# Kernel optimization log

Hardware: AMD Instinct MI355X
Metric: run time of the kernel (lower is better)

Reference implementation:

```python
import jax, jax.numpy as jnp
import numpy as np

B, N, H, E, OBS, A, AFF, EFF = 2, 50000, 64, 1_000_000, 128, 18, 512, 256


def setup_inputs() -> dict:
    key = jax.random.key(0)
    ks = jax.random.split(key, 20)
    s = 0.05  # small init to keep gates/tanh unsaturated
    return {
        "obs": jax.random.normal(ks[0], (B, OBS), jnp.float32),
        "state": jax.random.normal(ks[1], (B, N, H), jnp.float32) * 0.1,
        "W_in": jax.random.normal(ks[2], (OBS, H), jnp.float32) * s,
        "b_in": jnp.zeros((H,), jnp.float32),
        "W_msg": jax.random.normal(ks[3], (H, H), jnp.float32) * s,
        "W_gate": jax.random.normal(ks[4], (2 * H, H), jnp.float32) * s,
        "b_gate": jnp.zeros((H,), jnp.float32),
        "W_cand": jax.random.normal(ks[5], (2 * H, H), jnp.float32) * s,
        "b_cand": jnp.zeros((H,), jnp.float32),
        "W_dec": jax.random.normal(ks[6], (H, H), jnp.float32) * s,
        "b_dec": jnp.zeros((H,), jnp.float32),
        "W_mean": jax.random.normal(ks[7], (H, A), jnp.float32) * s,
        "b_mean": jnp.zeros((A,), jnp.float32),
        "W_ls": jax.random.normal(ks[8], (H, A), jnp.float32) * s,
        "b_ls": jnp.zeros((A,), jnp.float32),
        "src_index": jax.random.randint(ks[9], (E,), 0, N),
        "dst_index": jax.random.randint(ks[10], (E,), 0, N),
        "afferent_idx": jax.random.randint(ks[11], (AFF,), 0, N),
        "efferent_idx": jax.random.randint(ks[12], (EFF,), 0, N),
    }


def reference(obs, state, W_in, b_in, W_msg, W_gate, b_gate, W_cand, b_cand,
              W_dec, b_dec, W_mean, b_mean, W_ls, b_ls,
              src_index, dst_index, afferent_idx, efferent_idx):
    # inject obs projection into afferent node slots
    projected = obs @ W_in + b_in                                   # [B, H]
    injected = jnp.zeros_like(state).at[:, afferent_idx, :].set(projected[:, None, :])
    # gather-project-scatter message passing over the edge list
    src_msgs = state[:, src_index, :] @ W_msg                       # [B, E, H]
    messages = jnp.zeros_like(state).at[:, dst_index, :].add(src_msgs)
    # GRU-style gated update
    combined = messages + injected
    gate_in = jnp.concatenate([state, combined], axis=-1)           # [B, N, 2H]
    z = jax.nn.sigmoid(gate_in @ W_gate + b_gate)
    cand = jnp.tanh(gate_in @ W_cand + b_cand)
    next_state = (1.0 - z) * state + z * cand
    # mean-pool readout over efferent nodes, then policy heads
    readout = next_state[:, efferent_idx, :].mean(axis=1)           # [B, H]
    decoded = jnp.tanh(readout @ W_dec + b_dec)
    mean = decoded @ W_mean + b_mean
    log_std = jnp.clip(decoded @ W_ls + b_ls, -5.0, 2.0)
    return mean, log_std, next_state
```

## Files before the change

kernel.cpp:

```cpp
#include <hip/hip_runtime.h>
#include <hip/hip_bf16.h>

constexpr int kN   = 50000;
constexpr int kH   = 64;
constexpr int kB   = 2;
constexpr int kE   = 1000000;
constexpr int kObs = 128;
constexpr int kA   = 18;
constexpr int kAff = 512;
constexpr int kEff = 256;
constexpr int kNH  = kN * kH;
constexpr int kOutOff = 2 * kB * kA;
constexpr int kRanges = 8;
constexpr int kNr  = kN / kRanges;
constexpr int kChunks = 64;
constexpr int kEc  = kE / kChunks;
constexpr int kHistB = kRanges * kChunks;
constexpr int kPackBlocks = (kNH + 8191) / 8192;
constexpr int kWprepBlocks = 20;
constexpr int kScanB = (kN + 1023) / 1024;

typedef __attribute__((ext_vector_type(8))) short short8_t;
typedef __attribute__((ext_vector_type(4))) float f32x4_t;

__device__ __forceinline__ float ldf(const void* p, int i, int f32) {
  if (f32) return ((const float*)p)[i];
  unsigned short u = ((const unsigned short*)p)[i];
  union { unsigned int x; float f; } v; v.x = ((unsigned int)u) << 16; return v.f;
}
__device__ __forceinline__ void stf(void* p, int i, float val, int f32) {
  if (f32) ((float*)p)[i] = val;
  else ((__hip_bfloat16*)p)[i] = __float2bfloat16(val);
}
__device__ __forceinline__ float lo16(unsigned int w) {
  union { unsigned int i; float f; } v; v.i = w << 16; return v.f;
}
__device__ __forceinline__ float hi16(unsigned int w) {
  union { unsigned int i; float f; } v; v.i = w & 0xffff0000u; return v.f;
}
__device__ __forceinline__ unsigned int f2b(float f) {
  union { float f; unsigned int u; } v; v.f = f;
  unsigned int r = v.u + 0x7fffu + ((v.u >> 16) & 1u);
  return r >> 16;
}
__device__ __forceinline__ int detect64(const unsigned short* wprobe, int t) {
  int hits = 0;
  for (int k = 0; k < 4; ++k) {
    unsigned short u = wprobe[(t * 4 + k) * 2];
    int e = (u >> 7) & 0xFF;
    if ((u & 0x7FFFu) != 0 && e >= 108 && e <= 128) hits++;
  }
  for (int off = 32; off; off >>= 1) hits += __shfl_down(hits, off);
  return (hits < 128) ? 1 : 0;
}

extern "C" __global__ __launch_bounds__(1024) void k_prep(
    const unsigned short* __restrict__ wprobe,
    const void* __restrict__ obs,
    const void* __restrict__ W_in,
    const void* __restrict__ b_in,
    const int* __restrict__ aff_idx,
    const int* __restrict__ dst,
    const void* __restrict__ W_msg,
    const void* __restrict__ W_gate,
    const void* __restrict__ W_cand,
    int* __restrict__ dflag,
    int* __restrict__ flags,
    float* __restrict__ projected,
    int* __restrict__ deg_c,
    unsigned short* __restrict__ wt) {
  __shared__ int sdeg[kNr];
  int t = threadIdx.x, b = blockIdx.x;
  if (b == 0) {
    __shared__ int sflag;
    if (t < 64) { int f = detect64(wprobe, t); if (t == 0) { sflag = f; dflag[0] = f; } }
    __syncthreads();
    int f32 = sflag;
    if (t < kAff) flags[aff_idx[t]] = 1;
    if (t < kB * kH) {
      int bb = t >> 6, h = t & 63;
      float acc = ldf(b_in, h, f32);
      for (int o = 0; o < kObs; ++o)
        acc += ldf(obs, bb * kObs + o, f32) * ldf(W_in, o * kH + h, f32);
      projected[t] = acc;
    }
  } else if (b <= kHistB) {
    int h = b - 1, r = h & 7, c = h >> 3;
    int r0 = r * kNr;
    for (int i = t; i < kNr; i += 1024) sdeg[i] = 0;
    __syncthreads();
    int end = (c + 1) * kEc;
    for (int e = c * kEc + t; e < end; e += 1024) {
      unsigned rel = (unsigned)(dst[e] - r0);
      if (rel < (unsigned)kNr) atomicAdd(&sdeg[rel], 1);
    }
    __syncthreads();
    for (int i = t; i < kNr; i += 1024) deg_c[c * kN + r0 + i] = sdeg[i];
  } else {
    __shared__ int sflag;
    if (t < 64) { int f = detect64(wprobe, t); if (t == 0) sflag = f; }
    __syncthreads();
    int f32 = sflag;
    int i = (b - 1 - kHistB) * 1024 + t;
    if (i < 4096) {
      int n = i >> 6, k = i & 63;
      wt[i] = (unsigned short)f2b(ldf(W_msg, k * 64 + n, f32));
    } else if (i < 12288) {
      int j = i - 4096; int n = j >> 7, k = j & 127;
      wt[i] = (unsigned short)f2b(ldf(W_gate, k * 64 + n, f32));
    } else if (i < 20480) {
      int j = i - 12288; int n = j >> 7, k = j & 127;
      wt[i] = (unsigned short)f2b(ldf(W_cand, k * 64 + n, f32));
    }
  }
}

extern "C" __global__ void k_scan1(const int* __restrict__ deg_c,
                                   int* __restrict__ row_off,
                                   int* __restrict__ partials) {
  __shared__ int sd[256];
  int t = threadIdx.x;
  int base = blockIdx.x * 1024 + t * 4;
  int d[4];
#pragma unroll
  for (int k = 0; k < 4; ++k) {
    int idx = base + k, s = 0;
    if (idx < kN) {
      for (int r = 0; r < kChunks; ++r) s += deg_c[r * kN + idx];
    }
    d[k] = s;
  }
  int s4 = d[0] + d[1] + d[2] + d[3];
  sd[t] = s4;
  __syncthreads();
  for (int off = 1; off < 256; off <<= 1) {
    int v = (t >= off) ? sd[t - off] : 0;
    __syncthreads();
    sd[t] += v;
    __syncthreads();
  }
  int excl = sd[t] - s4;
  if (t == 255) partials[blockIdx.x] = sd[255];
#pragma unroll
  for (int k = 0; k < 4; ++k) {
    if (base + k < kN) row_off[base + k] = excl;
    excl += d[k];
  }
}

extern "C" __global__ void k_scan3(int* __restrict__ row_off,
                                   const int* __restrict__ partials,
                                   int* __restrict__ deg_c) {
  __shared__ int sd[256];
  int t = threadIdx.x;
  int chunk = blockIdx.x >> 2;
  int s = 0;
  for (int j = t; j < chunk; j += 256) s += partials[j];
  sd[t] = s;
  __syncthreads();
  for (int off = 128; off; off >>= 1) {
    if (t < off) sd[t] += sd[t + off];
    __syncthreads();
  }
  int base = sd[0];
  int i = blockIdx.x * 256 + t;
  if (i < kN) {
    int v = row_off[i] + base;
    row_off[i] = v;
    int run = v;
#pragma unroll 8
    for (int c = 0; c < kChunks; ++c) {
      int d = deg_c[c * kN + i];
      deg_c[c * kN + i] = run;
      run += d;
    }
  }
  if (blockIdx.x == 0 && t == 0) row_off[kN] = kE;
}

extern "C" __global__ __launch_bounds__(1024) void k_scatter(
    const int* __restrict__ src,
    const int* __restrict__ dst,
    const int* __restrict__ chunk_base,
    int* __restrict__ sorted_src,
    const unsigned short* __restrict__ wprobe,
    const void* __restrict__ state,
    unsigned int* __restrict__ pack) {
  __shared__ int scur[kNr];
  int t = threadIdx.x;
  if (blockIdx.x < kHistB) {
    int r = blockIdx.x & 7, c = blockIdx.x >> 3;
    int r0 = r * kNr;
    for (int i = t; i < kNr; i += 1024) scur[i] = chunk_base[c * kN + r0 + i];
    __syncthreads();
    int end = (c + 1) * kEc;
    for (int e = c * kEc + t; e < end; e += 1024) {
      unsigned rel = (unsigned)(dst[e] - r0);
      if (rel < (unsigned)kNr) {
        int pos = atomicAdd(&scur[rel], 1);
        sorted_src[pos] = src[e];
      }
    }
  } else {
    __shared__ int sflag;
    if (t < 64) { int f = detect64(wprobe, t); if (t == 0) sflag = f; }
    __syncthreads();
    int f32 = sflag;
    int i = (blockIdx.x - kHistB) * 8192 + t * 8;
    if (i < kNH) {
      uint4 o0, o1;
      if (!f32) {
        uint4 a = *(const uint4*)((const unsigned short*)state + i);
        uint4 c4 = *(const uint4*)((const unsigned short*)state + kNH + i);
        o0.x = (a.x & 0xffffu) | (c4.x << 16);
        o0.y = (a.x >> 16)     | (c4.x & 0xffff0000u);
        o0.z = (a.y & 0xffffu) | (c4.y << 16);
        o0.w = (a.y >> 16)     | (c4.y & 0xffff0000u);
        o1.x = (a.z & 0xffffu) | (c4.z << 16);
        o1.y = (a.z >> 16)     | (c4.z & 0xffff0000u);
        o1.z = (a.w & 0xffffu) | (c4.w << 16);
        o1.w = (a.w >> 16)     | (c4.w & 0xffff0000u);
      } else {
        const float* sf = (const float*)state;
        unsigned int w[8];
#pragma unroll
        for (int k = 0; k < 8; ++k)
          w[k] = f2b(sf[i + k]) | (f2b(sf[kNH + i + k]) << 16);
        o0 = make_uint4(w[0], w[1], w[2], w[3]);
        o1 = make_uint4(w[4], w[5], w[6], w[7]);
      }
      *(uint4*)&pack[i] = o0;
      *(uint4*)&pack[i + 4] = o1;
    }
  }
}

extern "C" __global__ __launch_bounds__(256) void k_gather(
    const unsigned int* __restrict__ pack,
    const int* __restrict__ row_off,
    const int* __restrict__ sorted_src,
    unsigned int* __restrict__ agg) {
  int wave = threadIdx.x >> 6, lane = threadIdx.x & 63;
  int n = blockIdx.x * 4 + wave;
  if (n >= kN) return;
  int s  = row_off[n];
  int en = row_off[n + 1];
  int g = lane >> 4, col = lane & 15;
  const uint4* pk4 = (const uint4*)pack;
  float a0x = 0.f, a0y = 0.f, a0z = 0.f, a0w = 0.f;
  float a1x = 0.f, a1y = 0.f, a1z = 0.f, a1w = 0.f;
  for (int e = s; e < en; e += 8) {
#pragma unroll
    for (int h = 0; h < 2; ++h) {
      int ee = e + h * 4 + g;
      int idx = sorted_src[min(ee, en - 1)];
      uint4 wv = pk4[idx * 16 + col];
      if (ee >= en) { wv.x = 0u; wv.y = 0u; wv.z = 0u; wv.w = 0u; }
      a0x += lo16(wv.x); a1x += hi16(wv.x);
      a0y += lo16(wv.y); a1y += hi16(wv.y);
      a0z += lo16(wv.z); a1z += hi16(wv.z);
      a0w += lo16(wv.w); a1w += hi16(wv.w);
    }
  }
  a0x += __shfl_xor(a0x, 16); a0x += __shfl_xor(a0x, 32);
  a0y += __shfl_xor(a0y, 16); a0y += __shfl_xor(a0y, 32);
  a0z += __shfl_xor(a0z, 16); a0z += __shfl_xor(a0z, 32);
  a0w += __shfl_xor(a0w, 16); a0w += __shfl_xor(a0w, 32);
  a1x += __shfl_xor(a1x, 16); a1x += __shfl_xor(a1x, 32);
  a1y += __shfl_xor(a1y, 16); a1y += __shfl_xor(a1y, 32);
  a1z += __shfl_xor(a1z, 16); a1z += __shfl_xor(a1z, 32);
  a1w += __shfl_xor(a1w, 16); a1w += __shfl_xor(a1w, 32);
  if (g == 0) {
    uint4 o;
    o.x = f2b(a0x) | (f2b(a1x) << 16);
    o.y = f2b(a0y) | (f2b(a1y) << 16);
    o.z = f2b(a0z) | (f2b(a1z) << 16);
    o.w = f2b(a0w) | (f2b(a1w) << 16);
    ((uint4*)agg)[n * 16 + col] = o;
  }
}

extern "C" __global__ __launch_bounds__(256) void k_update(
    const unsigned int* __restrict__ pk,
    const unsigned short* __restrict__ wt,
    const void* __restrict__ b_gate,
    const void* __restrict__ b_cand,
    const unsigned int* __restrict__ agg,
    const int* __restrict__ flags,
    const float* __restrict__ projected,
    const int* __restrict__ dflag,
    void* __restrict__ out) {
  __shared__ uint4 lw4[2752];
  __shared__ uint4 lx4[1088];
  __shared__ float sbias[128];
  __shared__ float sproj[128];
  __shared__ int   sfl[32];
  unsigned short* lwt = (unsigned short*)lw4;
  unsigned short* lx  = (unsigned short*)lx4;
  int f32 = dflag[0];
  int t = threadIdx.x;
  int nd0 = blockIdx.x * 32;

  const uint4* w4 = (const uint4*)wt;
  for (int i = t; i < 512; i += 256)  { int n = i >> 3, c = i & 7;  lw4[n * 9 + c] = w4[n * 8 + c]; }
  for (int i = t; i < 1024; i += 256) { int n = i >> 4, c = i & 15; lw4[576 + n * 17 + c] = w4[512 + n * 16 + c]; }
  for (int i = t; i < 1024; i += 256) { int n = i >> 4, c = i & 15; lw4[1664 + n * 17 + c] = w4[1536 + n * 16 + c]; }

  const uint4* pk4 = (const uint4*)pk;
  const uint4* ag4 = (const uint4*)agg;
  for (int i = t; i < 512; i += 256) {
    int ndl = i >> 4, c4 = i & 15;
    int ndg = min(nd0 + ndl, kN - 1);
    uint4 pv = pk4[ndg * 16 + c4];
    uint4 av = ag4[ndg * 16 + c4];
    *(uint2*)&lx[(2 * ndl) * 136 + c4 * 4] =
        make_uint2((pv.x & 0xffffu) | (pv.y << 16), (pv.z & 0xffffu) | (pv.w << 16));
    *(uint2*)&lx[(2 * ndl + 1) * 136 + c4 * 4] =
        make_uint2((pv.x >> 16) | (pv.y & 0xffff0000u), (pv.z >> 16) | (pv.w & 0xffff0000u));
    *(uint2*)&lx[(2 * ndl) * 136 + 64 + c4 * 4] =
        make_uint2((av.x & 0xffffu) | (av.y << 16), (av.z & 0xffffu) | (av.w << 16));
    *(uint2*)&lx[(2 * ndl + 1) * 136 + 64 + c4 * 4] =
        make_uint2((av.x >> 16) | (av.y & 0xffff0000u), (av.z >> 16) | (av.w & 0xffff0000u));
  }
  if (t < 64) sbias[t] = ldf(b_gate, t, f32);
  else if (t < 128) sbias[t] = ldf(b_cand, t - 64, f32);
  else sproj[t - 128] = projected[t - 128];
  if (t < 32) sfl[t] = (nd0 + t < kN) ? flags[nd0 + t] : 0;
  __syncthreads();

  int w = t >> 6, lane = t & 63;
  int q = lane >> 4, l15 = lane & 15;
  int rowb = w * 16;

  short8_t a0 = *(const short8_t*)&lx[(rowb + l15) * 136 + 64 + q * 8];
  short8_t a1 = *(const short8_t*)&lx[(rowb + l15) * 136 + 96 + q * 8];
  f32x4_t msgc[4];
#pragma unroll
  for (int ct = 0; ct < 4; ++ct) {
    f32x4_t acc = {0.f, 0.f, 0.f, 0.f};
    short8_t b0 = *(const short8_t*)&lwt[(ct * 16 + l15) * 72 + q * 8];
    short8_t b1 = *(const short8_t*)&lwt[(ct * 16 + l15) * 72 + 32 + q * 8];
    acc = __builtin_amdgcn_mfma_f32_16x16x32_bf16(a0, b0, acc, 0, 0, 0);
    acc = __builtin_amdgcn_mfma_f32_16x16x32_bf16(a1, b1, acc, 0, 0, 0);
    msgc[ct] = acc;
  }
#pragma unroll
  for (int ct = 0; ct < 4; ++ct) {
    int col = ct * 16 + l15;
    float pj0 = sproj[col], pj1 = sproj[64 + col];
#pragma unroll
    for (int r = 0; r < 4; ++r) {
      int row = rowb + q * 4 + r;
      int ndl = row >> 1, b = row & 1;
      float inj = sfl[ndl] ? (b ? pj1 : pj0) : 0.f;
      lx[row * 136 + 64 + col] = (unsigned short)f2b(msgc[ct][r] + inj);
    }
  }

  short8_t xa[4];
#pragma unroll
  for (int ks = 0; ks < 4; ++ks)
    xa[ks] = *(const short8_t*)&lx[(rowb + l15) * 136 + ks * 32 + q * 8];
#pragma unroll
  for (int ct = 0; ct < 4; ++ct) {
    f32x4_t accg = {0.f, 0.f, 0.f, 0.f}, accc = {0.f, 0.f, 0.f, 0.f};
#pragma unroll
    for (int ks = 0; ks < 4; ++ks) {
      short8_t bg = *(const short8_t*)&lwt[4608 + (ct * 16 + l15) * 136 + ks * 32 + q * 8];
      short8_t bc = *(const short8_t*)&lwt[13312 + (ct * 16 + l15) * 136 + ks * 32 + q * 8];
      accg = __builtin_amdgcn_mfma_f32_16x16x32_bf16(xa[ks], bg, accg, 0, 0, 0);
      accc = __builtin_amdgcn_mfma_f32_16x16x32_bf16(xa[ks], bc, accc, 0, 0, 0);
    }
    int col = ct * 16 + l15;
    float bgv = sbias[col], bcv = sbias[64 + col];
#pragma unroll
    for (int rp = 0; rp < 2; ++rp) {
      int rowe = rowb + q * 4 + 2 * rp;
      int nd = nd0 + (rowe >> 1);
      if (nd >= kN) continue;
      unsigned int pv = pk[nd * 64 + col];
      float z0 = 1.f / (1.f + __expf(-(accg[2 * rp] + bgv)));
      float c0 = tanhf(accc[2 * rp] + bcv);
      stf(out, kOutOff + nd * 64 + col, (1.f - z0) * lo16(pv) + z0 * c0, f32);
      float z1 = 1.f / (1.f + __expf(-(accg[2 * rp + 1] + bgv)));
      float c1 = tanhf(accc[2 * rp + 1] + bcv);
      stf(out, kOutOff + kNH + nd * 64 + col, (1.f - z1) * hi16(pv) + z1 * c1, f32);
    }
  }
}

extern "C" __global__ void k_readout(const void* __restrict__ W_dec,
                                     const void* __restrict__ b_dec,
                                     const void* __restrict__ W_mean,
                                     const void* __restrict__ b_mean,
                                     const void* __restrict__ W_ls,
                                     const void* __restrict__ b_ls,
                                     const int* __restrict__ eff_idx,
                                     const int* __restrict__ dflag,
                                     void* __restrict__ out) {
  __shared__ float part[8][64];
  __shared__ float ro[128], dec[128];
  int f32 = dflag[0];
  int t = threadIdx.x;
  int wv = t >> 6, lane = t & 63;
  int b = wv >> 2, g = wv & 3;
  float acc = 0.f;
#pragma unroll 4
  for (int i = 0; i < 64; ++i) {
    int n = eff_idx[g * 64 + i];
    acc += ldf(out, kOutOff + b * kNH + n * 64 + lane, f32);
  }
  part[wv][lane] = acc;
  __syncthreads();
  if (t < 128) {
    int bb = t >> 6, h = t & 63;
    float s = part[bb * 4 + 0][h] + part[bb * 4 + 1][h] +
              part[bb * 4 + 2][h] + part[bb * 4 + 3][h];
    ro[t] = s * (1.f / kEff);
  }
  __syncthreads();
  if (t < 128) {
    int bb = t >> 6, h = t & 63;
    float d = ldf(b_dec, h, f32);
    for (int k = 0; k < 64; ++k) d += ro[bb * 64 + k] * ldf(W_dec, k * 64 + h, f32);
    dec[t] = tanhf(d);
  }
  __syncthreads();
  if (t < kB * kA) {
    int bb = t / kA, a = t % kA;
    float m = ldf(b_mean, a, f32), l = ldf(b_ls, a, f32);
    for (int k = 0; k < 64; ++k) {
      float dv = dec[bb * 64 + k];
      m += dv * ldf(W_mean, k * kA + a, f32);
      l += dv * ldf(W_ls, k * kA + a, f32);
    }
    l = fminf(fmaxf(l, -5.f), 2.f);
    stf(out, t, m, f32);
    stf(out, kB * kA + t, l, f32);
  }
}

extern "C" void kernel_launch(void* const* d_in, const int* in_sizes, int n_in,
                              void* d_out, int out_size, void* d_ws, size_t ws_size,
                              hipStream_t stream) {
  (void)in_sizes; (void)n_in; (void)out_size; (void)ws_size;
  const void* obs    = d_in[0];
  const void* state  = d_in[1];
  const void* W_in   = d_in[2];
  const void* b_in   = d_in[3];
  const void* W_msg  = d_in[4];
  const void* W_gate = d_in[5];
  const void* b_gate = d_in[6];
  const void* W_cand = d_in[7];
  const void* b_cand = d_in[8];
  const void* W_dec  = d_in[9];
  const void* b_dec  = d_in[10];
  const void* W_mean = d_in[11];
  const void* b_mean = d_in[12];
  const void* W_ls   = d_in[13];
  const void* b_ls   = d_in[14];
  const int* src = (const int*)d_in[15];
  const int* dst = (const int*)d_in[16];
  const int* aff = (const int*)d_in[17];
  const int* eff = (const int*)d_in[18];

  int* wsp        = (int*)d_ws;
  int* flags      = wsp;
  int* deg_c      = flags + kN;
  int* row_off    = deg_c + kChunks * kN;
  int* partials   = row_off + (kN + 64);
  int* dflag      = partials + 512;
  float* projected = (float*)(dflag + 16);
  int* sorted_src  = (int*)(projected + 128);
  unsigned int* pk  = (unsigned int*)(sorted_src + kE);
  unsigned int* agg = pk + kNH;
  unsigned short* wt = (unsigned short*)(agg + kNH);

  hipMemsetAsync(flags, 0, size_t(kN) * sizeof(int), stream);
  k_prep<<<1 + kHistB + kWprepBlocks, 1024, 0, stream>>>(
      (const unsigned short*)W_cand, obs, W_in, b_in, aff, dst,
      W_msg, W_gate, W_cand, dflag, flags, projected, deg_c, wt);
  k_scan1<<<kScanB, 256, 0, stream>>>(deg_c, row_off, partials);
  k_scan3<<<(kN + 255) / 256, 256, 0, stream>>>(row_off, partials, deg_c);
  k_scatter<<<kHistB + kPackBlocks, 1024, 0, stream>>>(
      src, dst, deg_c, sorted_src, (const unsigned short*)W_cand, state, pk);
  k_gather<<<(kN + 3) / 4, 256, 0, stream>>>(pk, row_off, sorted_src, agg);
  k_update<<<(kN + 31) / 32, 256, 0, stream>>>(pk, wt, b_gate, b_cand,
                                               agg, flags, projected, dflag, d_out);
  k_readout<<<1, 512, 0, stream>>>(W_dec, b_dec, W_mean, b_mean, W_ls, b_ls, eff,
                                   dflag, d_out);
}
```

Baseline: 285.5 us.

## Fold flag memset into prep, widen scan1 grid, read update weights from global

Three changes. The flags memset is removed and the zeroing is done inside block 0 of k_prep, saving one launch. k_scan1 now uses one node per thread over four times as many blocks, which spreads the column sums over more parallelism, and k_scan3 indexes partials per block to match. k_update no longer stages the weight matrices in LDS and reads MFMA B operands directly from global/L2, cutting LDS use and staging time per block at the cost of unpadded global reads.

```diff
diff --git a/kernel.cpp b/kernel.cpp
--- a/kernel.cpp
+++ b/kernel.cpp
@@ -18,7 +18,7 @@
 constexpr int kHistB = kRanges * kChunks;
 constexpr int kPackBlocks = (kNH + 8191) / 8192;
 constexpr int kWprepBlocks = 20;
-constexpr int kScanB = (kN + 1023) / 1024;
+constexpr int kScanB = (kN + 255) / 256;
 
 typedef __attribute__((ext_vector_type(8))) short short8_t;
 typedef __attribute__((ext_vector_type(4))) float f32x4_t;
@@ -74,6 +74,7 @@
   if (b == 0) {
     __shared__ int sflag;
     if (t < 64) { int f = detect64(wprobe, t); if (t == 0) { sflag = f; dflag[0] = f; } }
+    for (int i = t; i < kN; i += 1024) flags[i] = 0;
     __syncthreads();
     int f32 = sflag;
     if (t < kAff) flags[aff_idx[t]] = 1;
@@ -120,18 +121,12 @@
                                    int* __restrict__ partials) {
   __shared__ int sd[256];
   int t = threadIdx.x;
-  int base = blockIdx.x * 1024 + t * 4;
-  int d[4];
-#pragma unroll
-  for (int k = 0; k < 4; ++k) {
-    int idx = base + k, s = 0;
-    if (idx < kN) {
-      for (int r = 0; r < kChunks; ++r) s += deg_c[r * kN + idx];
-    }
-    d[k] = s;
-  }
-  int s4 = d[0] + d[1] + d[2] + d[3];
-  sd[t] = s4;
+  int n = blockIdx.x * 256 + t;
+  int s = 0;
+  if (n < kN) {
+    for (int c = 0; c < kChunks; ++c) s += deg_c[c * kN + n];
+  }
+  sd[t] = s;
   __syncthreads();
   for (int off = 1; off < 256; off <<= 1) {
     int v = (t >= off) ? sd[t - off] : 0;
@@ -139,13 +134,9 @@
     sd[t] += v;
     __syncthreads();
   }
-  int excl = sd[t] - s4;
+  int excl = sd[t] - s;
   if (t == 255) partials[blockIdx.x] = sd[255];
-#pragma unroll
-  for (int k = 0; k < 4; ++k) {
-    if (base + k < kN) row_off[base + k] = excl;
-    excl += d[k];
-  }
+  if (n < kN) row_off[n] = excl;
 }
 
 extern "C" __global__ void k_scan3(int* __restrict__ row_off,
@@ -153,9 +144,8 @@
                                    int* __restrict__ deg_c) {
   __shared__ int sd[256];
   int t = threadIdx.x;
-  int chunk = blockIdx.x >> 2;
   int s = 0;
-  for (int j = t; j < chunk; j += 256) s += partials[j];
+  for (int j = t; j < (int)blockIdx.x; j += 256) s += partials[j];
   sd[t] = s;
   __syncthreads();
   for (int off = 128; off; off >>= 1) {
@@ -163,15 +153,15 @@
     __syncthreads();
   }
   int base = sd[0];
-  int i = blockIdx.x * 256 + t;
-  if (i < kN) {
-    int v = row_off[i] + base;
-    row_off[i] = v;
+  int n = blockIdx.x * 256 + t;
+  if (n < kN) {
+    int v = row_off[n] + base;
+    row_off[n] = v;
     int run = v;
 #pragma unroll 8
     for (int c = 0; c < kChunks; ++c) {
-      int d = deg_c[c * kN + i];
-      deg_c[c * kN + i] = run;
+      int d = deg_c[c * kN + n];
+      deg_c[c * kN + n] = run;
       run += d;
     }
   }
@@ -290,21 +280,14 @@
     const float* __restrict__ projected,
     const int* __restrict__ dflag,
     void* __restrict__ out) {
-  __shared__ uint4 lw4[2752];
   __shared__ uint4 lx4[1088];
   __shared__ float sbias[128];
   __shared__ float sproj[128];
   __shared__ int   sfl[32];
-  unsigned short* lwt = (unsigned short*)lw4;
   unsigned short* lx  = (unsigned short*)lx4;
   int f32 = dflag[0];
   int t = threadIdx.x;
   int nd0 = blockIdx.x * 32;
-
-  const uint4* w4 = (const uint4*)wt;
-  for (int i = t; i < 512; i += 256)  { int n = i >> 3, c = i & 7;  lw4[n * 9 + c] = w4[n * 8 + c]; }
-  for (int i = t; i < 1024; i += 256) { int n = i >> 4, c = i & 15; lw4[576 + n * 17 + c] = w4[512 + n * 16 + c]; }
-  for (int i = t; i < 1024; i += 256) { int n = i >> 4, c = i & 15; lw4[1664 + n * 17 + c] = w4[1536 + n * 16 + c]; }
 
   const uint4* pk4 = (const uint4*)pk;
   const uint4* ag4 = (const uint4*)agg;
@@ -331,6 +314,9 @@
   int w = t >> 6, lane = t & 63;
   int q = lane >> 4, l15 = lane & 15;
   int rowb = w * 16;
+  const unsigned short* wm = wt;
+  const unsigned short* wg = wt + 4096;
+  const unsigned short* wc = wt + 12288;
 
   short8_t a0 = *(const short8_t*)&lx[(rowb + l15) * 136 + 64 + q * 8];
   short8_t a1 = *(const short8_t*)&lx[(rowb + l15) * 136 + 96 + q * 8];
@@ -338,8 +324,8 @@
 #pragma unroll
   for (int ct = 0; ct < 4; ++ct) {
     f32x4_t acc = {0.f, 0.f, 0.f, 0.f};
-    short8_t b0 = *(const short8_t*)&lwt[(ct * 16 + l15) * 72 + q * 8];
-    short8_t b1 = *(const short8_t*)&lwt[(ct * 16 + l15) * 72 + 32 + q * 8];
+    short8_t b0 = *(const short8_t*)&wm[(ct * 16 + l15) * 64 + q * 8];
+    short8_t b1 = *(const short8_t*)&wm[(ct * 16 + l15) * 64 + 32 + q * 8];
     acc = __builtin_amdgcn_mfma_f32_16x16x32_bf16(a0, b0, acc, 0, 0, 0);
     acc = __builtin_amdgcn_mfma_f32_16x16x32_bf16(a1, b1, acc, 0, 0, 0);
     msgc[ct] = acc;
@@ -366,8 +352,8 @@
     f32x4_t accg = {0.f, 0.f, 0.f, 0.f}, accc = {0.f, 0.f, 0.f, 0.f};
 #pragma unroll
     for (int ks = 0; ks < 4; ++ks) {
-      short8_t bg = *(const short8_t*)&lwt[4608 + (ct * 16 + l15) * 136 + ks * 32 + q * 8];
-      short8_t bc = *(const short8_t*)&lwt[13312 + (ct * 16 + l15) * 136 + ks * 32 + q * 8];
+      short8_t bg = *(const short8_t*)&wg[(ct * 16 + l15) * 128 + ks * 32 + q * 8];
+      short8_t bc = *(const short8_t*)&wc[(ct * 16 + l15) * 128 + ks * 32 + q * 8];
       accg = __builtin_amdgcn_mfma_f32_16x16x32_bf16(xa[ks], bg, accg, 0, 0, 0);
       accc = __builtin_amdgcn_mfma_f32_16x16x32_bf16(xa[ks], bc, accc, 0, 0, 0);
     }
@@ -476,12 +462,11 @@
   unsigned int* agg = pk + kNH;
   unsigned short* wt = (unsigned short*)(agg + kNH);
 
-  hipMemsetAsync(flags, 0, size_t(kN) * sizeof(int), stream);
   k_prep<<<1 + kHistB + kWprepBlocks, 1024, 0, stream>>>(
       (const unsigned short*)W_cand, obs, W_in, b_in, aff, dst,
       W_msg, W_gate, W_cand, dflag, flags, projected, deg_c, wt);
   k_scan1<<<kScanB, 256, 0, stream>>>(deg_c, row_off, partials);
-  k_scan3<<<(kN + 255) / 256, 256, 0, stream>>>(row_off, partials, deg_c);
+  k_scan3<<<kScanB, 256, 0, stream>>>(row_off, partials, deg_c);
   k_scatter<<<kHistB + kPackBlocks, 1024, 0, stream>>>(
       src, dst, deg_c, sorted_src, (const unsigned short*)W_cand, state, pk);
   k_gather<<<(kN + 3) / 4, 256, 0, stream>>>(pk, row_off, sorted_src, agg);
```

Measured after the change: 281.1 us. No clear change (-1.5%).
